# Kernel tuning notes

Measured on AMD Instinct MI355X. Metric: run time of the kernel, lower is better.

Reference implementation:

```python
import jax, jax.numpy as jnp
import numpy as np

HIDDEN = 2048
HEADS = 16
HEAD_DIM = HIDDEN // HEADS
BATCH = 2
SEQ = 2048


def setup_inputs() -> dict:
    key = jax.random.key(0)
    ks = jax.random.split(key, 9)
    s = 0.02
    return {
        "x": jax.random.normal(ks[0], (BATCH, SEQ, HIDDEN), dtype=jnp.float32),
        "Wq": jax.random.normal(ks[1], (HIDDEN, HIDDEN), dtype=jnp.float32) * s,
        "bq": jax.random.normal(ks[2], (HIDDEN,), dtype=jnp.float32) * s,
        "Wk": jax.random.normal(ks[3], (HIDDEN, HIDDEN), dtype=jnp.float32) * s,
        "bk": jax.random.normal(ks[4], (HIDDEN,), dtype=jnp.float32) * s,
        "Wv": jax.random.normal(ks[5], (HIDDEN, HIDDEN), dtype=jnp.float32) * s,
        "bv": jax.random.normal(ks[6], (HIDDEN,), dtype=jnp.float32) * s,
        "Wo": jax.random.normal(ks[7], (HIDDEN, HIDDEN), dtype=jnp.float32) * s,
        "bo": jax.random.normal(ks[8], (HIDDEN,), dtype=jnp.float32) * s,
    }


def reference(x, Wq, bq, Wk, bk, Wv, bv, Wo, bo):
    B, S, H = x.shape
    # Linear layers: y = x @ W.T + b (torch nn.Linear convention, W:[out,in])
    q = x @ Wq.T + bq
    k = x @ Wk.T + bk
    v = x @ Wv.T + bv
    # [B, S, H] -> [B, nH, S, hd]
    def split_heads(t):
        return t.reshape(B, S, HEADS, HEAD_DIM).transpose(0, 2, 1, 3)
    q, k, v = split_heads(q), split_heads(k), split_heads(v)
    scale = 1.0 / (HEAD_DIM ** 0.5)
    # NOTE: original module applies NO causal mask despite its name; be faithful.
    scores = jnp.einsum('bhqd,bhkd->bhqk', q, k) * scale
    probs = jax.nn.softmax(scores, axis=-1)
    attn = jnp.einsum('bhqk,bhkd->bhqd', probs, v)
    attn = attn.transpose(0, 2, 1, 3).reshape(B, S, H)
    return attn @ Wo.T + bo
```

## Files before the change

### kernel.cpp

```cpp
#include <hip/hip_runtime.h>
#include <hip/hip_bf16.h>
#include <stdint.h>

typedef __bf16 bf16_t;
typedef __attribute__((ext_vector_type(8))) __bf16 bf16x8;
typedef __attribute__((ext_vector_type(4))) float floatx4;
typedef __attribute__((ext_vector_type(16))) float f32x16;

typedef __attribute__((address_space(1))) const unsigned int gu32_t;
typedef __attribute__((address_space(3))) unsigned int lu32_t;

__device__ __forceinline__ void async16(const void* g, void* l) {
    __builtin_amdgcn_global_load_lds((gu32_t*)g, (lu32_t*)l, 16, 0, 0);
}

__device__ __forceinline__ uint32_t pack2(float lo, float hi) {
    union { bf16_t h[2]; uint32_t u; } cv;
    cv.h[0] = (bf16_t)lo; cv.h[1] = (bf16_t)hi;
    return cv.u;
}

__global__ __launch_bounds__(256) void cvt_f32_bf16(const float* __restrict__ in,
                                                    bf16_t* __restrict__ out) {
    int i = (blockIdx.x * 256 + threadIdx.x) * 8;
    float4 a = *(const float4*)(in + i);
    float4 b = *(const float4*)(in + i + 4);
    bf16x8 v;
    v[0] = (bf16_t)a.x; v[1] = (bf16_t)a.y; v[2] = (bf16_t)a.z; v[3] = (bf16_t)a.w;
    v[4] = (bf16_t)b.x; v[5] = (bf16_t)b.y; v[6] = (bf16_t)b.z; v[7] = (bf16_t)b.w;
    *(bf16x8*)(out + i) = v;
}

template <bool OUT_F32, bool BIAS_ROW>
__global__ __launch_bounds__(256) void gemm_bt(const bf16_t* __restrict__ A,
                                               const bf16_t* __restrict__ B,
                                               const float* __restrict__ bias,
                                               const float* __restrict__ bias2,
                                               int nsplit,
                                               float* __restrict__ Cf,
                                               bf16_t* __restrict__ Cb,
                                               int M, int N, int K, int ldc) {
    __shared__ bf16_t As[128 * 64];
    __shared__ bf16_t Bs[128 * 64];
    const int tid = threadIdx.x;
    const int wave = tid >> 6, lane = tid & 63;
    const int quad = lane >> 4, l16 = lane & 15;
    const int wm = (wave >> 1) * 64, wn = (wave & 1) * 64;
    const int tm = blockIdx.x * 128, tn = blockIdx.y * 128;

    floatx4 acc[4][4];
#pragma unroll
    for (int i = 0; i < 4; ++i)
#pragma unroll
        for (int j = 0; j < 4; ++j) acc[i][j] = floatx4{0.f, 0.f, 0.f, 0.f};

    const bf16_t* Abase = A + (size_t)tm * K;
    const bf16_t* Bbase = B + (size_t)tn * K;
    const int sw = l16 & 7;

    for (int kk = 0; kk < K; kk += 64) {
#pragma unroll
        for (int it = 0; it < 4; ++it) {
            int chunk = it * 256 + tid;
            int r = chunk >> 3, c = chunk & 7;
            int c2 = c ^ (r & 7);
            async16(Abase + r * K + kk + c2 * 8, As + (it * 256 + wave * 64) * 8);
            async16(Bbase + r * K + kk + c2 * 8, Bs + (it * 256 + wave * 64) * 8);
        }
        __syncthreads();
#pragma unroll
        for (int ks = 0; ks < 2; ++ks) {
            bf16x8 af[4], bf[4];
#pragma unroll
            for (int mt = 0; mt < 4; ++mt)
                af[mt] = *(const bf16x8*)(As + (wm + mt * 16 + l16) * 64 +
                                          ((ks * 4 + quad) ^ sw) * 8);
#pragma unroll
            for (int nt = 0; nt < 4; ++nt)
                bf[nt] = *(const bf16x8*)(Bs + (wn + nt * 16 + l16) * 64 +
                                          ((ks * 4 + quad) ^ sw) * 8);
#pragma unroll
            for (int mt = 0; mt < 4; ++mt)
#pragma unroll
                for (int nt = 0; nt < 4; ++nt)
                    acc[mt][nt] = __builtin_amdgcn_mfma_f32_16x16x32_bf16(af[mt], bf[nt],
                                                                          acc[mt][nt], 0, 0, 0);
        }
        __syncthreads();
    }
#pragma unroll
    for (int mt = 0; mt < 4; ++mt)
#pragma unroll
        for (int nt = 0; nt < 4; ++nt)
#pragma unroll
            for (int r = 0; r < 4; ++r) {
                int row = tm + wm + mt * 16 + quad * 4 + r;
                int col = tn + wn + nt * 16 + l16;
                float bv = BIAS_ROW ? bias[row]
                                    : (col < nsplit ? bias[col] : bias2[col - nsplit]);
                float v = acc[mt][nt][r] + bv;
                if (OUT_F32) Cf[(size_t)row * ldc + col] = v;
                else Cb[(size_t)row * ldc + col] = (bf16_t)v;
            }
}

__global__ __launch_bounds__(128, 2) void flash_attn(const bf16_t* __restrict__ Qp,
                                                     const bf16_t* __restrict__ Kp,
                                                     const bf16_t* __restrict__ Vt,
                                                     bf16_t* __restrict__ O) {
    __shared__ bf16_t Ks[64 * 128];
    __shared__ bf16_t Vts[128 * 64];
    const int tid = threadIdx.x;
    const int wv = tid >> 6, lane = tid & 63;
    const int hi = lane >> 5, l32 = lane & 31;
    const int LD = 4096, T = 4096, S = 2048, HO = 2048;
    const float SL2E = 0.088388347688f * 1.44269504089f;

    const int qrow0 = blockIdx.z * S + blockIdx.x * 64;
    const int krow0 = blockIdx.z * S;
    const int hoff = blockIdx.y * 128;
    const int sw7 = l32 & 7;

    bf16x8 qf[8];
    const bf16_t* qptr = Qp + (size_t)(qrow0 + wv * 32 + l32) * LD + hoff + hi * 8;
#pragma unroll
    for (int ks = 0; ks < 8; ++ks) qf[ks] = *(const bf16x8*)(qptr + ks * 16);

    float m_i = -3.0e38f, l_i = 0.f;
    f32x16 Oacc[4];
#pragma unroll
    for (int dt = 0; dt < 4; ++dt)
#pragma unroll
        for (int r = 0; r < 16; ++r) Oacc[dt][r] = 0.f;

    for (int kt = 0; kt < 32; ++kt) {
        int kb = krow0 + kt * 64;
#pragma unroll
        for (int it = 0; it < 8; ++it) {
            int chunk = it * 128 + tid;
            int r = chunk >> 4, c = chunk & 15;
            int c2 = c ^ (r & 7);
            async16(Kp + (size_t)(kb + r) * LD + hoff + c2 * 8, Ks + chunk * 8);
        }
#pragma unroll
        for (int it = 0; it < 8; ++it) {
            int chunk = it * 128 + tid;
            int r = chunk >> 3, c = chunk & 7;
            int c2 = c ^ (r & 7);
            async16(Vt + (size_t)(hoff + r) * T + kb + c2 * 8, Vts + chunk * 8);
        }
        __syncthreads();

        f32x16 sf[2];
#pragma unroll
        for (int mt = 0; mt < 2; ++mt)
#pragma unroll
            for (int r = 0; r < 16; ++r) sf[mt][r] = 0.f;
#pragma unroll
        for (int ks = 0; ks < 8; ++ks) {
#pragma unroll
            for (int mt = 0; mt < 2; ++mt) {
                bf16x8 a = *(const bf16x8*)(Ks + (mt * 32 + l32) * 128 +
                                            ((2 * ks + hi) ^ sw7) * 8);
                sf[mt] = __builtin_amdgcn_mfma_f32_32x32x16_bf16(a, qf[ks], sf[mt], 0, 0, 0);
            }
        }

        float mx = -3.0e38f;
#pragma unroll
        for (int mt = 0; mt < 2; ++mt)
#pragma unroll
            for (int r = 0; r < 16; ++r) mx = fmaxf(mx, sf[mt][r]);
        mx = fmaxf(mx, __shfl_xor(mx, 32));
        mx *= SL2E;
        float mnew = fmaxf(m_i, mx);
        float alpha = exp2f(m_i - mnew);
        m_i = mnew;

        float rsum = 0.f;
        uint32_t pk[16];
#pragma unroll
        for (int mt = 0; mt < 2; ++mt)
#pragma unroll
            for (int a4 = 0; a4 < 4; ++a4) {
                float p0 = exp2f(sf[mt][4 * a4 + 0] * SL2E - mnew);
                float p1 = exp2f(sf[mt][4 * a4 + 1] * SL2E - mnew);
                float p2 = exp2f(sf[mt][4 * a4 + 2] * SL2E - mnew);
                float p3 = exp2f(sf[mt][4 * a4 + 3] * SL2E - mnew);
                rsum += (p0 + p1) + (p2 + p3);
                pk[mt * 8 + a4 * 2 + 0] = pack2(p0, p1);
                pk[mt * 8 + a4 * 2 + 1] = pack2(p2, p3);
            }
        rsum += __shfl_xor(rsum, 32);
        l_i = l_i * alpha + rsum;

#pragma unroll
        for (int dt = 0; dt < 4; ++dt)
#pragma unroll
            for (int r = 0; r < 16; ++r) Oacc[dt][r] *= alpha;

#pragma unroll
        for (int s = 0; s < 4; ++s) {
            int base = (s >> 1) * 8 + (s & 1) * 4;
            uint32_t PA0 = pk[base + 0], PA1 = pk[base + 1];
            uint32_t PB0 = pk[base + 2], PB1 = pk[base + 3];
            uint32_t rA0 = (uint32_t)__shfl_xor((int)PA0, 32);
            uint32_t rA1 = (uint32_t)__shfl_xor((int)PA1, 32);
            uint32_t rB0 = (uint32_t)__shfl_xor((int)PB0, 32);
            uint32_t rB1 = (uint32_t)__shfl_xor((int)PB1, 32);
            union { uint32_t u[4]; bf16x8 v; } w;
            w.u[0] = hi ? rB0 : PA0;
            w.u[1] = hi ? rB1 : PA1;
            w.u[2] = hi ? PB0 : rA0;
            w.u[3] = hi ? PB1 : rA1;
#pragma unroll
            for (int dt = 0; dt < 4; ++dt) {
                bf16x8 a = *(const bf16x8*)(Vts + (dt * 32 + l32) * 64 +
                                            ((2 * s + hi) ^ sw7) * 8);
                Oacc[dt] = __builtin_amdgcn_mfma_f32_32x32x16_bf16(a, w.v, Oacc[dt], 0, 0, 0);
            }
        }
        __syncthreads();
    }

    float linv = 1.0f / l_i;
    uint32_t* Os = (uint32_t*)Ks + wv * 2048;
#pragma unroll
    for (int dt = 0; dt < 4; ++dt)
#pragma unroll
        for (int a4 = 0; a4 < 4; ++a4) {
            uint32_t q0 = pack2(Oacc[dt][4 * a4 + 0] * linv, Oacc[dt][4 * a4 + 1] * linv);
            uint32_t q1 = pack2(Oacc[dt][4 * a4 + 2] * linv, Oacc[dt][4 * a4 + 3] * linv);
            int d2 = 16 * dt + 4 * a4 + 2 * hi;
            Os[l32 * 64 + ((d2 + 2 * l32) & 63)] = q0;
            Os[l32 * 64 + ((d2 + 1 + 2 * l32) & 63)] = q1;
        }
#pragma unroll
    for (int r = 0; r < 32; ++r) {
        uint32_t v = Os[r * 64 + ((lane + 2 * r) & 63)];
        uint32_t* orow = (uint32_t*)(O + (size_t)(qrow0 + wv * 32 + r) * HO + hoff);
        orow[lane] = v;
    }
}

extern "C" void kernel_launch(void* const* d_in, const int* in_sizes, int n_in,
                              void* d_out, int out_size, void* d_ws, size_t ws_size,
                              hipStream_t stream) {
    const float* x  = (const float*)d_in[0];
    const float* Wq = (const float*)d_in[1];
    const float* bq = (const float*)d_in[2];
    const float* Wk = (const float*)d_in[3];
    const float* bk = (const float*)d_in[4];
    const float* Wv = (const float*)d_in[5];
    const float* bv = (const float*)d_in[6];
    const float* Wo = (const float*)d_in[7];
    const float* bo = (const float*)d_in[8];
    float* out = (float*)d_out;

    const int T = 4096;
    const int H = 2048;
    bf16_t* ws  = (bf16_t*)d_ws;
    bf16_t* xb  = ws;
    bf16_t* wqb = xb  + (size_t)T * H;
    bf16_t* wkb = wqb + (size_t)H * H;
    bf16_t* wvb = wkb + (size_t)H * H;
    bf16_t* wob = wvb + (size_t)H * H;
    bf16_t* QKb = wob + (size_t)H * H;
    bf16_t* Vtb = QKb + (size_t)T * 2 * H;
    bf16_t* Ab  = Vtb + (size_t)H * T;
    size_t need = (size_t)(Ab + (size_t)T * H - ws) * sizeof(bf16_t);
    if (ws_size < need) return;

    cvt_f32_bf16<<<T * H / 2048, 256, 0, stream>>>(x, xb);
    cvt_f32_bf16<<<H * H / 2048, 256, 0, stream>>>(Wq, wqb);
    cvt_f32_bf16<<<H * H / 2048, 256, 0, stream>>>(Wk, wkb);
    cvt_f32_bf16<<<H * H / 2048, 256, 0, stream>>>(Wv, wvb);
    cvt_f32_bf16<<<H * H / 2048, 256, 0, stream>>>(Wo, wob);

    dim3 gqk(T / 128, 4096 / 128);
    gemm_bt<false, false><<<gqk, 256, 0, stream>>>(xb, wqb, bq, bk, H,
                                                   nullptr, QKb, T, 4096, H, 4096);
    dim3 gv(H / 128, T / 128);
    gemm_bt<false, true><<<gv, 256, 0, stream>>>(wvb, xb, bv, nullptr, 0,
                                                 nullptr, Vtb, H, T, H, T);

    flash_attn<<<dim3(32, 16, 2), 128, 0, stream>>>(QKb, QKb + H, Vtb, Ab);

    dim3 go(T / 128, H / 128);
    gemm_bt<true, false><<<go, 256, 0, stream>>>(Ab, wob, bo, nullptr, H,
                                                 out, nullptr, T, H, H, H);
}
```

Measured before the change: 463.0 us.

## Split attention key tiles across wave pairs and merge partial softmax states

Flash attention blocks go from 2 to 4 waves. Each pair of waves shares a 32-row query slice and each wave handles half of every 64-key tile, so per-wave register pressure drops and more waves fit per CU. At the end, running max and sum are exchanged through shared memory and the partial outputs are combined in LDS before being written out. This adds extra synchronisation, a reduction epilogue, and duplicated Q fragment loads per wave pair.

```diff
diff --git a/kernel.cpp b/kernel.cpp
--- a/kernel.cpp
+++ b/kernel.cpp
@@ -104,15 +104,17 @@
             }
 }
 
-__global__ __launch_bounds__(128, 2) void flash_attn(const bf16_t* __restrict__ Qp,
+__global__ __launch_bounds__(256, 4) void flash_attn(const bf16_t* __restrict__ Qp,
                                                      const bf16_t* __restrict__ Kp,
                                                      const bf16_t* __restrict__ Vt,
                                                      bf16_t* __restrict__ O) {
-    __shared__ bf16_t Ks[64 * 128];
-    __shared__ bf16_t Vts[128 * 64];
+    __shared__ bf16_t smem[64 * 128 + 128 * 64];
+    bf16_t* Ks = smem;
+    bf16_t* Vts = smem + 64 * 128;
     const int tid = threadIdx.x;
     const int wv = tid >> 6, lane = tid & 63;
     const int hi = lane >> 5, l32 = lane & 31;
+    const int wq = wv >> 1, wk = wv & 1;
     const int LD = 4096, T = 4096, S = 2048, HO = 2048;
     const float SL2E = 0.088388347688f * 1.44269504089f;
 
@@ -122,7 +124,7 @@
     const int sw7 = l32 & 7;
 
     bf16x8 qf[8];
-    const bf16_t* qptr = Qp + (size_t)(qrow0 + wv * 32 + l32) * LD + hoff + hi * 8;
+    const bf16_t* qptr = Qp + (size_t)(qrow0 + wq * 32 + l32) * LD + hoff + hi * 8;
 #pragma unroll
     for (int ks = 0; ks < 8; ++ks) qf[ks] = *(const bf16x8*)(qptr + ks * 16);
 
@@ -136,41 +138,34 @@
     for (int kt = 0; kt < 32; ++kt) {
         int kb = krow0 + kt * 64;
 #pragma unroll
-        for (int it = 0; it < 8; ++it) {
-            int chunk = it * 128 + tid;
+        for (int it = 0; it < 4; ++it) {
+            int chunk = it * 256 + tid;
             int r = chunk >> 4, c = chunk & 15;
             int c2 = c ^ (r & 7);
             async16(Kp + (size_t)(kb + r) * LD + hoff + c2 * 8, Ks + chunk * 8);
         }
 #pragma unroll
-        for (int it = 0; it < 8; ++it) {
-            int chunk = it * 128 + tid;
+        for (int it = 0; it < 4; ++it) {
+            int chunk = it * 256 + tid;
             int r = chunk >> 3, c = chunk & 7;
             int c2 = c ^ (r & 7);
             async16(Vt + (size_t)(hoff + r) * T + kb + c2 * 8, Vts + chunk * 8);
         }
         __syncthreads();
 
-        f32x16 sf[2];
-#pragma unroll
-        for (int mt = 0; mt < 2; ++mt)
-#pragma unroll
-            for (int r = 0; r < 16; ++r) sf[mt][r] = 0.f;
+        f32x16 sf;
+#pragma unroll
+        for (int r = 0; r < 16; ++r) sf[r] = 0.f;
 #pragma unroll
         for (int ks = 0; ks < 8; ++ks) {
-#pragma unroll
-            for (int mt = 0; mt < 2; ++mt) {
-                bf16x8 a = *(const bf16x8*)(Ks + (mt * 32 + l32) * 128 +
-                                            ((2 * ks + hi) ^ sw7) * 8);
-                sf[mt] = __builtin_amdgcn_mfma_f32_32x32x16_bf16(a, qf[ks], sf[mt], 0, 0, 0);
-            }
+            bf16x8 a = *(const bf16x8*)(Ks + (wk * 32 + l32) * 128 +
+                                        ((2 * ks + hi) ^ sw7) * 8);
+            sf = __builtin_amdgcn_mfma_f32_32x32x16_bf16(a, qf[ks], sf, 0, 0, 0);
         }
 
         float mx = -3.0e38f;
 #pragma unroll
-        for (int mt = 0; mt < 2; ++mt)
-#pragma unroll
-            for (int r = 0; r < 16; ++r) mx = fmaxf(mx, sf[mt][r]);
+        for (int r = 0; r < 16; ++r) mx = fmaxf(mx, sf[r]);
         mx = fmaxf(mx, __shfl_xor(mx, 32));
         mx *= SL2E;
         float mnew = fmaxf(m_i, mx);
@@ -178,19 +173,17 @@
         m_i = mnew;
 
         float rsum = 0.f;
-        uint32_t pk[16];
-#pragma unroll
-        for (int mt = 0; mt < 2; ++mt)
-#pragma unroll
-            for (int a4 = 0; a4 < 4; ++a4) {
-                float p0 = exp2f(sf[mt][4 * a4 + 0] * SL2E - mnew);
-                float p1 = exp2f(sf[mt][4 * a4 + 1] * SL2E - mnew);
-                float p2 = exp2f(sf[mt][4 * a4 + 2] * SL2E - mnew);
-                float p3 = exp2f(sf[mt][4 * a4 + 3] * SL2E - mnew);
-                rsum += (p0 + p1) + (p2 + p3);
-                pk[mt * 8 + a4 * 2 + 0] = pack2(p0, p1);
-                pk[mt * 8 + a4 * 2 + 1] = pack2(p2, p3);
-            }
+        uint32_t pk[8];
+#pragma unroll
+        for (int a4 = 0; a4 < 4; ++a4) {
+            float p0 = exp2f(sf[4 * a4 + 0] * SL2E - mnew);
+            float p1 = exp2f(sf[4 * a4 + 1] * SL2E - mnew);
+            float p2 = exp2f(sf[4 * a4 + 2] * SL2E - mnew);
+            float p3 = exp2f(sf[4 * a4 + 3] * SL2E - mnew);
+            rsum += (p0 + p1) + (p2 + p3);
+            pk[a4 * 2 + 0] = pack2(p0, p1);
+            pk[a4 * 2 + 1] = pack2(p2, p3);
+        }
         rsum += __shfl_xor(rsum, 32);
         l_i = l_i * alpha + rsum;
 
@@ -200,46 +193,84 @@
             for (int r = 0; r < 16; ++r) Oacc[dt][r] *= alpha;
 
 #pragma unroll
-        for (int s = 0; s < 4; ++s) {
-            int base = (s >> 1) * 8 + (s & 1) * 4;
-            uint32_t PA0 = pk[base + 0], PA1 = pk[base + 1];
-            uint32_t PB0 = pk[base + 2], PB1 = pk[base + 3];
-            uint32_t rA0 = (uint32_t)__shfl_xor((int)PA0, 32);
-            uint32_t rA1 = (uint32_t)__shfl_xor((int)PA1, 32);
-            uint32_t rB0 = (uint32_t)__shfl_xor((int)PB0, 32);
-            uint32_t rB1 = (uint32_t)__shfl_xor((int)PB1, 32);
+        for (int s = 0; s < 2; ++s) {
+            uint32_t r0 = (uint32_t)__shfl_xor((int)pk[4 * s + 0], 32);
+            uint32_t r1 = (uint32_t)__shfl_xor((int)pk[4 * s + 1], 32);
+            uint32_t r2 = (uint32_t)__shfl_xor((int)pk[4 * s + 2], 32);
+            uint32_t r3 = (uint32_t)__shfl_xor((int)pk[4 * s + 3], 32);
             union { uint32_t u[4]; bf16x8 v; } w;
-            w.u[0] = hi ? rB0 : PA0;
-            w.u[1] = hi ? rB1 : PA1;
-            w.u[2] = hi ? PB0 : rA0;
-            w.u[3] = hi ? PB1 : rA1;
+            w.u[0] = hi ? r2 : pk[4 * s + 0];
+            w.u[1] = hi ? r3 : pk[4 * s + 1];
+            w.u[2] = hi ? pk[4 * s + 2] : r0;
+            w.u[3] = hi ? pk[4 * s + 3] : r1;
 #pragma unroll
             for (int dt = 0; dt < 4; ++dt) {
                 bf16x8 a = *(const bf16x8*)(Vts + (dt * 32 + l32) * 64 +
-                                            ((2 * s + hi) ^ sw7) * 8);
+                                            ((4 * wk + 2 * s + hi) ^ sw7) * 8);
                 Oacc[dt] = __builtin_amdgcn_mfma_f32_32x32x16_bf16(a, w.v, Oacc[dt], 0, 0, 0);
             }
         }
         __syncthreads();
     }
 
-    float linv = 1.0f / l_i;
-    uint32_t* Os = (uint32_t*)Ks + wv * 2048;
+    float* ml = (float*)smem;
+    if (hi == 0) {
+        ml[wv * 64 + l32] = m_i;
+        ml[wv * 64 + 32 + l32] = l_i;
+    }
+    __syncthreads();
+    float m_o = ml[(wv ^ 1) * 64 + l32];
+    float l_o = ml[(wv ^ 1) * 64 + 32 + l32];
+    float mfin = fmaxf(m_i, m_o);
+    float a_s = exp2f(m_i - mfin);
+    float a_o = exp2f(m_o - mfin);
+    float linv = 1.0f / (l_i * a_s + l_o * a_o);
 #pragma unroll
     for (int dt = 0; dt < 4; ++dt)
 #pragma unroll
-        for (int a4 = 0; a4 < 4; ++a4) {
-            uint32_t q0 = pack2(Oacc[dt][4 * a4 + 0] * linv, Oacc[dt][4 * a4 + 1] * linv);
-            uint32_t q1 = pack2(Oacc[dt][4 * a4 + 2] * linv, Oacc[dt][4 * a4 + 3] * linv);
-            int d2 = 16 * dt + 4 * a4 + 2 * hi;
-            Os[l32 * 64 + ((d2 + 2 * l32) & 63)] = q0;
-            Os[l32 * 64 + ((d2 + 1 + 2 * l32) & 63)] = q1;
-        }
-#pragma unroll
-    for (int r = 0; r < 32; ++r) {
-        uint32_t v = Os[r * 64 + ((lane + 2 * r) & 63)];
-        uint32_t* orow = (uint32_t*)(O + (size_t)(qrow0 + wv * 32 + r) * HO + hoff);
-        orow[lane] = v;
+        for (int r = 0; r < 16; ++r) Oacc[dt][r] *= a_s;
+    __syncthreads();
+
+    float* Op = (float*)smem;
+    if (wk == 1) {
+#pragma unroll
+        for (int dt = 0; dt < 4; ++dt)
+#pragma unroll
+            for (int r = 0; r < 16; ++r) {
+                int d = dt * 32 + (r & 3) + 8 * (r >> 2) + 4 * hi;
+                Op[(wq * 128 + d) * 32 + l32] = Oacc[dt][r];
+            }
+    }
+    __syncthreads();
+    if (wk == 0) {
+#pragma unroll
+        for (int dt = 0; dt < 4; ++dt)
+#pragma unroll
+            for (int r = 0; r < 16; ++r) {
+                int d = dt * 32 + (r & 3) + 8 * (r >> 2) + 4 * hi;
+                Oacc[dt][r] = (Oacc[dt][r] + Op[(wq * 128 + d) * 32 + l32]) * linv;
+            }
+    }
+    __syncthreads();
+
+    if (wk == 0) {
+        uint32_t* Os = (uint32_t*)smem + wq * 2048;
+#pragma unroll
+        for (int dt = 0; dt < 4; ++dt)
+#pragma unroll
+            for (int a4 = 0; a4 < 4; ++a4) {
+                uint32_t q0 = pack2(Oacc[dt][4 * a4 + 0], Oacc[dt][4 * a4 + 1]);
+                uint32_t q1 = pack2(Oacc[dt][4 * a4 + 2], Oacc[dt][4 * a4 + 3]);
+                int d2 = 16 * dt + 4 * a4 + 2 * hi;
+                Os[l32 * 64 + ((d2 + 2 * l32) & 63)] = q0;
+                Os[l32 * 64 + ((d2 + 1 + 2 * l32) & 63)] = q1;
+            }
+#pragma unroll
+        for (int r = 0; r < 32; ++r) {
+            uint32_t v = Os[r * 64 + ((lane + 2 * r) & 63)];
+            uint32_t* orow = (uint32_t*)(O + (size_t)(qrow0 + wq * 32 + r) * HO + hoff);
+            orow[lane] = v;
+        }
     }
 }
 
@@ -284,7 +315,7 @@
     gemm_bt<false, true><<<gv, 256, 0, stream>>>(wvb, xb, bv, nullptr, 0,
                                                  nullptr, Vtb, H, T, H, T);
 
-    flash_attn<<<dim3(32, 16, 2), 128, 0, stream>>>(QKb, QKb + H, Vtb, Ab);
+    flash_attn<<<dim3(32, 16, 2), 256, 0, stream>>>(QKb, QKb + H, Vtb, Ab);
 
     dim3 go(T / 128, H / 128);
     gemm_bt<true, false><<<go, 256, 0, stream>>>(Ab, wob, bo, nullptr, H,
```

Result: slower. 532.3 us (+15.0%).
